# Kernel tuning notes

Hardware: AMD Instinct MI355X
Metric: run time of the kernel (lower is better)

Reference implementation:

```python
import jax, jax.numpy as jnp
import numpy as np

RES = (64, 64)
TEMP = 0.1  # forward default temp

def _mgrid(res):
    # matches torch.meshgrid(linspace(0, r-1, r)...) with default 'ij' indexing
    gs = jnp.meshgrid(*[jnp.arange(r, dtype=jnp.float32) for r in res], indexing='ij')
    return jnp.stack(gs, 0)  # [2, H, W]

def setup_inputs() -> dict:
    key = jax.random.key(0)
    k1, k2 = jax.random.split(key)
    x = jax.random.normal(k1, (8, 32, RES[0], RES[1]), dtype=jnp.float32)
    of = jax.random.normal(k2, (8, 2, RES[0], RES[1]), dtype=jnp.float32)
    return {"x": x, "of": of}

def reference(x, of):
    bs, C = x.shape[0], x.shape[1]
    hw = RES[0] * RES[1]
    gpos = _mgrid(RES).reshape(2, hw)                 # [2, HW] target pixel positions
    opos = gpos[None] + of.reshape(bs, 2, hw)         # [bs, 2, HW] flow-displaced source positions
    # L1 distance: logits[b, i, j] = sum_c |opos[b, c, j] - gpos[c, i]|
    dist = jnp.abs(opos[:, :, None, :] - gpos[None, :, :, None]).sum(axis=1)  # [bs, HW, HW]
    # softmax over target axis i (dim=-2 in torch) -> each source pixel j distributes mass over targets
    locs = jax.nn.softmax(-dist / TEMP, axis=1)       # [bs, HW, HW]
    # out[b, c, i] = sum_j x[b, c, j] * locs[b, i, j]
    out = jnp.einsum('bij,bcj->bci', locs, x.reshape(bs, C, hw))
    return out.reshape(bs, C, RES[0], RES[1])
```

## Files before the change

kernel.cpp:

```cpp
#include <hip/hip_runtime.h>
#include <hip/hip_fp16.h>
#include <math.h>

#define HW    4096
#define NC    32
#define NB    8
#define TINV  10.0f
#define RWIN  8
#define WDIM  (8 + 2 * RWIN)
#define RCUT  2.0f


__device__ __forceinline__ __half2 u32_as_h2(unsigned int u) {
    union { unsigned int u; __half2 h; } c; c.u = u; return c.h;
}
__device__ __forceinline__ unsigned int h2_as_u32(__half2 h) {
    union { __half2 h; unsigned int u; } c; c.h = h; return c.u;
}

__global__ __launch_bounds__(256) void prep_kernel(
    const float* __restrict__ x, const float* __restrict__ of,
    float4* __restrict__ params, __half2* __restrict__ xt2)
{
    __shared__ float tile[16][257];
    int bx   = blockIdx.x;
    int half = blockIdx.y;
    int b    = bx >> 4;
    int j0   = (bx & 15) << 8;
    int t    = threadIdx.x;
    int j    = j0 + t;
    int ch0  = half << 4;

    if (half == 0) {
        float oy = (float)(j >> 6) + of[(b * 2 + 0) * HW + j];
        float ox = (float)(j & 63) + of[(b * 2 + 1) * HW + j];
        int cy0 = min(max((int)floorf(oy), 0), 63);
        int cx0 = min(max((int)floorf(ox), 0), 63);
        float Dy = 0.f, Dx = 0.f;
        #pragma unroll
        for (int d = -3; d <= 3; ++d) {
            int iy = cy0 + d, ix = cx0 + d;
            if ((unsigned)iy < 64u) Dy += __expf(-TINV * fabsf(oy - (float)iy));
            if ((unsigned)ix < 64u) Dx += __expf(-TINV * fabsf(ox - (float)ix));
        }
        params[(b << 12) + j] = make_float4(oy, ox, 1.f / Dy, 1.f / Dx);
    }

    #pragma unroll
    for (int c = 0; c < 16; ++c)
        tile[c][t] = x[((b * NC + ch0 + c) << 12) + j];
    __syncthreads();
    #pragma unroll
    for (int k = 0; k < 8; ++k) {
        int o   = k * 256 + t;
        int jj  = o >> 3, pr = o & 7;
        xt2[((size_t)((b << 12) + j0 + jj)) * 16 + (half << 3) + pr] =
            __floats2half2_rn(tile[2 * pr][jj], tile[2 * pr + 1][jj]);
    }
}

__global__ __launch_bounds__(256) void gather_kernel(
    const float4* __restrict__ params, const unsigned int* __restrict__ xtu,
    float* __restrict__ out)
{
    __shared__ float4       wp[4][65];
    __shared__ int          sj[4][64];
    __shared__ unsigned int pool[4 * 64 * 9];

    const int b    = blockIdx.z;
    const int h    = blockIdx.y;
    const int tile = blockIdx.x;
    const int ty0  = (tile >> 3) << 3;
    const int tx0  = (tile & 7) << 3;

    const int tid  = threadIdx.x;
    const int lane = tid & 63;
    const int wv   = __builtin_amdgcn_readfirstlane(tid >> 6);

    const float iy = (float)(ty0 + (lane >> 3));
    const float ix = (float)(tx0 + (lane & 7));

    __half2 acc8[8];
    #pragma unroll
    for (int c = 0; c < 8; ++c) acc8[c] = __floats2half2_rn(0.f, 0.f);

    const float4*       pb = params + (b << 12);
    const unsigned int* xb = xtu + (size_t)(b << 12) * 16 + (h << 3);

    const int srow = lane >> 5;
    const int scol = lane & 31;

    unsigned int* XSu = pool;

    for (int r = 0; r < 3; ++r) {
        int ry = wv + srow * 4 + r * 8;
        int jy = ty0 - RWIN + ry;
        int jx = tx0 - RWIN + scol;
        bool valid = ((unsigned)jy < 64u) && ((unsigned)jx < 64u) && (scol < WDIM);
        int j = (jy << 6) + jx;
        float4 p = pb[valid ? j : 0];
        float cy = fminf(fmaxf(p.x, 0.f), 63.f);
        float cx = fminf(fmaxf(p.y, 0.f), 63.f);
        float dyr = fmaxf(fmaxf((float)ty0 - cy, cy - ((float)ty0 + 7.f)), 0.f);
        float dxr = fmaxf(fmaxf((float)tx0 - cx, cx - ((float)tx0 + 7.f)), 0.f);
        bool pred = valid && (dyr + dxr < RCUT);

        unsigned long long m = __ballot(pred);
        int cnt = __popcll(m);
        if (pred) {
            int pos = __builtin_amdgcn_mbcnt_hi((unsigned)(m >> 32),
                      __builtin_amdgcn_mbcnt_lo((unsigned)m, 0u));
            wp[wv][pos] = p;
            sj[wv][pos] = j;
        }
        if (lane == cnt) wp[wv][cnt] = make_float4(1.f, 1.f, 0.f, 0.f);
        int cntp = cnt + (cnt & 1);

        for (int m4 = 0; m4 < cntp; m4 += 32) {
            int s = m4 + (lane >> 1);
            if (s < cntp) {
                int jj = sj[wv][min(s, cnt - 1)];
                const uint4* src = (const uint4*)(xb + jj * 16 + ((lane & 1) << 2));
                *(uint4*)&XSu[(((wv << 6) + s) << 3) + ((lane & 1) << 2)] = *src;
            }
        }

        for (int k = 0; k < cntp; k += 2) {
            float4 p0 = wp[wv][k], p1 = wp[wv][k + 1];
            const uint4* x0 = (const uint4*)&XSu[((wv << 6) + k)     << 3];
            const uint4* x1 = (const uint4*)&XSu[((wv << 6) + k + 1) << 3];
            uint4 A0 = x0[0], A1 = x0[1];
            uint4 B0 = x1[0], B1 = x1[1];

            float g0 = (__expf(-TINV * fabsf(p0.x - iy)) * p0.z)
                     * (__expf(-TINV * fabsf(p0.y - ix)) * p0.w);
            float g1 = (__expf(-TINV * fabsf(p1.x - iy)) * p1.z)
                     * (__expf(-TINV * fabsf(p1.y - ix)) * p1.w);
            __half2 hg0 = __float2half2_rn(g0);
            __half2 hg1 = __float2half2_rn(g1);

            acc8[0] = __hfma2(hg0, u32_as_h2(A0.x), acc8[0]);
            acc8[1] = __hfma2(hg0, u32_as_h2(A0.y), acc8[1]);
            acc8[2] = __hfma2(hg0, u32_as_h2(A0.z), acc8[2]);
            acc8[3] = __hfma2(hg0, u32_as_h2(A0.w), acc8[3]);
            acc8[4] = __hfma2(hg0, u32_as_h2(A1.x), acc8[4]);
            acc8[5] = __hfma2(hg0, u32_as_h2(A1.y), acc8[5]);
            acc8[6] = __hfma2(hg0, u32_as_h2(A1.z), acc8[6]);
            acc8[7] = __hfma2(hg0, u32_as_h2(A1.w), acc8[7]);

            acc8[0] = __hfma2(hg1, u32_as_h2(B0.x), acc8[0]);
            acc8[1] = __hfma2(hg1, u32_as_h2(B0.y), acc8[1]);
            acc8[2] = __hfma2(hg1, u32_as_h2(B0.z), acc8[2]);
            acc8[3] = __hfma2(hg1, u32_as_h2(B0.w), acc8[3]);
            acc8[4] = __hfma2(hg1, u32_as_h2(B1.x), acc8[4]);
            acc8[5] = __hfma2(hg1, u32_as_h2(B1.y), acc8[5]);
            acc8[6] = __hfma2(hg1, u32_as_h2(B1.z), acc8[6]);
            acc8[7] = __hfma2(hg1, u32_as_h2(B1.w), acc8[7]);
        }
    }

    __syncthreads();
    unsigned int* redu = pool;
    unsigned int* myr  = redu + ((wv << 6) + lane) * 9;
    #pragma unroll
    for (int c = 0; c < 8; ++c) myr[c] = h2_as_u32(acc8[c]);
    __syncthreads();

    int c2  = tid >> 5;
    int t32 = tid & 31;
    #pragma unroll
    for (int k = 0; k < 2; ++k) {
        int t = t32 + 32 * k;
        float sx = 0.f, sy = 0.f;
        #pragma unroll
        for (int w = 0; w < 4; ++w) {
            float2 f = __half22float2(u32_as_h2(redu[((w << 6) + t) * 9 + c2]));
            sx += f.x; sy += f.y;
        }
        int ch   = h * 16 + 2 * c2;
        int base = (((b << 5) + ch) << 12) + (ty0 + (t >> 3)) * 64 + (tx0 + (t & 7));
        out[base]        = sx;
        out[base + 4096] = sy;
    }
}

extern "C" void kernel_launch(void* const* d_in, const int* in_sizes, int n_in,
                              void* d_out, int out_size, void* d_ws, size_t ws_size,
                              hipStream_t stream) {
    const float* x  = (const float*)d_in[0];
    const float* of = (const float*)d_in[1];
    float* out = (float*)d_out;

    float4*  params = (float4*)d_ws;
    __half2* xt2    = (__half2*)((char*)d_ws + NB * HW * sizeof(float4));

    prep_kernel<<<dim3(NB * 16, 2), dim3(256), 0, stream>>>(x, of, params, xt2);
    gather_kernel<<<dim3(64, 2, NB), dim3(256), 0, stream>>>(
        params, (const unsigned int*)xt2, out);
}
```

Before: 67.85 us.

## Fuse prep into gather kernel, staging source window params and fp16 x in LDS

Removes the separate prep kernel and global workspace. Each gather block now computes flow params for its 24x24 source window and loads and converts the window's x channels to half2 directly into shared memory. The per-wave global gather is replaced by indexed LDS reads. This saves one launch and a global round-trip, at the cost of redundant param/exp computation and x loads across overlapping windows, plus more LDS per block, which may lower occupancy.

Result: slower. 73.47 us (+8.3%).

```diff
diff --git a/kernel.cpp b/kernel.cpp
--- a/kernel.cpp
+++ b/kernel.cpp
@@ -8,6 +8,7 @@
 #define TINV  10.0f
 #define RWIN  8
 #define WDIM  (8 + 2 * RWIN)
+#define NSRC  (WDIM * WDIM)
 #define RCUT  2.0f
 
 
@@ -18,64 +19,68 @@
     union { __half2 h; unsigned int u; } c; c.h = h; return c.u;
 }
 
-__global__ __launch_bounds__(256) void prep_kernel(
+__global__ __launch_bounds__(256) void warp_fused_kernel(
     const float* __restrict__ x, const float* __restrict__ of,
-    float4* __restrict__ params, __half2* __restrict__ xt2)
-{
-    __shared__ float tile[16][257];
-    int bx   = blockIdx.x;
-    int half = blockIdx.y;
-    int b    = bx >> 4;
-    int j0   = (bx & 15) << 8;
-    int t    = threadIdx.x;
-    int j    = j0 + t;
-    int ch0  = half << 4;
-
-    if (half == 0) {
-        float oy = (float)(j >> 6) + of[(b * 2 + 0) * HW + j];
-        float ox = (float)(j & 63) + of[(b * 2 + 1) * HW + j];
-        int cy0 = min(max((int)floorf(oy), 0), 63);
-        int cx0 = min(max((int)floorf(ox), 0), 63);
-        float Dy = 0.f, Dx = 0.f;
-        #pragma unroll
-        for (int d = -3; d <= 3; ++d) {
-            int iy = cy0 + d, ix = cx0 + d;
-            if ((unsigned)iy < 64u) Dy += __expf(-TINV * fabsf(oy - (float)iy));
-            if ((unsigned)ix < 64u) Dx += __expf(-TINV * fabsf(ox - (float)ix));
-        }
-        params[(b << 12) + j] = make_float4(oy, ox, 1.f / Dy, 1.f / Dx);
-    }
-
-    #pragma unroll
-    for (int c = 0; c < 16; ++c)
-        tile[c][t] = x[((b * NC + ch0 + c) << 12) + j];
-    __syncthreads();
-    #pragma unroll
-    for (int k = 0; k < 8; ++k) {
-        int o   = k * 256 + t;
-        int jj  = o >> 3, pr = o & 7;
-        xt2[((size_t)((b << 12) + j0 + jj)) * 16 + (half << 3) + pr] =
-            __floats2half2_rn(tile[2 * pr][jj], tile[2 * pr + 1][jj]);
-    }
-}
-
-__global__ __launch_bounds__(256) void gather_kernel(
-    const float4* __restrict__ params, const unsigned int* __restrict__ xtu,
     float* __restrict__ out)
 {
+    __shared__ float4       pw[NSRC];
+    __shared__ unsigned int xw[NSRC * 8];
     __shared__ float4       wp[4][65];
     __shared__ int          sj[4][64];
-    __shared__ unsigned int pool[4 * 64 * 9];
 
     const int b    = blockIdx.z;
     const int h    = blockIdx.y;
     const int tile = blockIdx.x;
     const int ty0  = (tile >> 3) << 3;
     const int tx0  = (tile & 7) << 3;
-
     const int tid  = threadIdx.x;
     const int lane = tid & 63;
     const int wv   = __builtin_amdgcn_readfirstlane(tid >> 6);
+
+    for (int s = tid; s < NSRC; s += 256) {
+        int wr = s / WDIM, wc = s - wr * WDIM;
+        int jy = ty0 - RWIN + wr, jx = tx0 - RWIN + wc;
+        float4 pv = make_float4(0.f, 0.f, 0.f, 0.f);
+        if (((unsigned)jy < 64u) && ((unsigned)jx < 64u)) {
+            int j = (jy << 6) + jx;
+            float oy = (float)jy + of[(b * 2 + 0) * HW + j];
+            float ox = (float)jx + of[(b * 2 + 1) * HW + j];
+            int cy0 = min(max((int)floorf(oy), 0), 63);
+            int cx0 = min(max((int)floorf(ox), 0), 63);
+            float Dy = 0.f, Dx = 0.f;
+            #pragma unroll
+            for (int d = -3; d <= 3; ++d) {
+                int iy2 = cy0 + d, ix2 = cx0 + d;
+                if ((unsigned)iy2 < 64u) Dy += __expf(-TINV * fabsf(oy - (float)iy2));
+                if ((unsigned)ix2 < 64u) Dx += __expf(-TINV * fabsf(ox - (float)ix2));
+            }
+            pv = make_float4(oy, ox, 1.f / Dy, 1.f / Dx);
+        }
+        pw[s] = pv;
+    }
+
+    const float* xb = x + ((size_t)((b * NC) + (h << 4)) << 12);
+    for (int i = tid; i < 8 * WDIM * 6; i += 256) {
+        int pr  = i / (WDIM * 6);
+        int rem = i - pr * (WDIM * 6);
+        int row = rem / 6, seg = rem - row * 6;
+        int jy  = ty0 - RWIN + row;
+        int jx0 = tx0 - RWIN + (seg << 2);
+        unsigned int q0 = 0, q1 = 0, q2 = 0, q3 = 0;
+        if (((unsigned)jy < 64u) && ((unsigned)jx0 < 61u)) {
+            const float* src = xb + ((2 * pr) << 12) + (jy << 6) + jx0;
+            float4 a = *(const float4*)src;
+            float4 c = *(const float4*)(src + HW);
+            q0 = h2_as_u32(__floats2half2_rn(a.x, c.x));
+            q1 = h2_as_u32(__floats2half2_rn(a.y, c.y));
+            q2 = h2_as_u32(__floats2half2_rn(a.z, c.z));
+            q3 = h2_as_u32(__floats2half2_rn(a.w, c.w));
+        }
+        unsigned int* d = &xw[((row * WDIM + (seg << 2)) << 3) + pr];
+        d[0] = q0; d[8] = q1; d[16] = q2; d[24] = q3;
+    }
+
+    __syncthreads();
 
     const float iy = (float)(ty0 + (lane >> 3));
     const float ix = (float)(tx0 + (lane & 7));
@@ -84,21 +89,16 @@
     #pragma unroll
     for (int c = 0; c < 8; ++c) acc8[c] = __floats2half2_rn(0.f, 0.f);
 
-    const float4*       pb = params + (b << 12);
-    const unsigned int* xb = xtu + (size_t)(b << 12) * 16 + (h << 3);
-
     const int srow = lane >> 5;
     const int scol = lane & 31;
-
-    unsigned int* XSu = pool;
 
     for (int r = 0; r < 3; ++r) {
         int ry = wv + srow * 4 + r * 8;
         int jy = ty0 - RWIN + ry;
         int jx = tx0 - RWIN + scol;
         bool valid = ((unsigned)jy < 64u) && ((unsigned)jx < 64u) && (scol < WDIM);
-        int j = (jy << 6) + jx;
-        float4 p = pb[valid ? j : 0];
+        int ws = ry * WDIM + min(scol, WDIM - 1);
+        float4 p = pw[ws];
         float cy = fminf(fmaxf(p.x, 0.f), 63.f);
         float cx = fminf(fmaxf(p.y, 0.f), 63.f);
         float dyr = fmaxf(fmaxf((float)ty0 - cy, cy - ((float)ty0 + 7.f)), 0.f);
@@ -111,24 +111,15 @@
             int pos = __builtin_amdgcn_mbcnt_hi((unsigned)(m >> 32),
                       __builtin_amdgcn_mbcnt_lo((unsigned)m, 0u));
             wp[wv][pos] = p;
-            sj[wv][pos] = j;
+            sj[wv][pos] = ws;
         }
-        if (lane == cnt) wp[wv][cnt] = make_float4(1.f, 1.f, 0.f, 0.f);
+        if (lane == cnt) { wp[wv][cnt] = make_float4(1.f, 1.f, 0.f, 0.f); sj[wv][cnt] = 0; }
         int cntp = cnt + (cnt & 1);
-
-        for (int m4 = 0; m4 < cntp; m4 += 32) {
-            int s = m4 + (lane >> 1);
-            if (s < cntp) {
-                int jj = sj[wv][min(s, cnt - 1)];
-                const uint4* src = (const uint4*)(xb + jj * 16 + ((lane & 1) << 2));
-                *(uint4*)&XSu[(((wv << 6) + s) << 3) + ((lane & 1) << 2)] = *src;
-            }
-        }
 
         for (int k = 0; k < cntp; k += 2) {
             float4 p0 = wp[wv][k], p1 = wp[wv][k + 1];
-            const uint4* x0 = (const uint4*)&XSu[((wv << 6) + k)     << 3];
-            const uint4* x1 = (const uint4*)&XSu[((wv << 6) + k + 1) << 3];
+            const uint4* x0 = (const uint4*)&xw[sj[wv][k]     << 3];
+            const uint4* x1 = (const uint4*)&xw[sj[wv][k + 1] << 3];
             uint4 A0 = x0[0], A1 = x0[1];
             uint4 B0 = x1[0], B1 = x1[1];
 
@@ -160,7 +151,7 @@
     }
 
     __syncthreads();
-    unsigned int* redu = pool;
+    unsigned int* redu = (unsigned int*)pw;
     unsigned int* myr  = redu + ((wv << 6) + lane) * 9;
     #pragma unroll
     for (int c = 0; c < 8; ++c) myr[c] = h2_as_u32(acc8[c]);
@@ -177,10 +168,10 @@
             float2 f = __half22float2(u32_as_h2(redu[((w << 6) + t) * 9 + c2]));
             sx += f.x; sy += f.y;
         }
-        int ch   = h * 16 + 2 * c2;
+        int ch   = (h << 4) + 2 * c2;
         int base = (((b << 5) + ch) << 12) + (ty0 + (t >> 3)) * 64 + (tx0 + (t & 7));
-        out[base]        = sx;
-        out[base + 4096] = sy;
+        out[base]      = sx;
+        out[base + HW] = sy;
     }
 }
 
@@ -190,11 +181,7 @@
     const float* x  = (const float*)d_in[0];
     const float* of = (const float*)d_in[1];
     float* out = (float*)d_out;
+    (void)d_ws; (void)ws_size;
 
-    float4*  params = (float4*)d_ws;
-    __half2* xt2    = (__half2*)((char*)d_ws + NB * HW * sizeof(float4));
-
-    prep_kernel<<<dim3(NB * 16, 2), dim3(256), 0, stream>>>(x, of, params, xt2);
-    gather_kernel<<<dim3(64, 2, NB), dim3(256), 0, stream>>>(
-        params, (const unsigned int*)xt2, out);
+    warp_fused_kernel<<<dim3(64, 2, NB), dim3(256), 0, stream>>>(x, of, out);
 }
```
